# Performance work log

Measured on AMD Instinct MI355X. Metric: run time of the kernel, lower is better.

## Reference

```python
import jax, jax.numpy as jnp
import numpy as np

C = 256
INTER = 32  # C // reduction_ratio(8)
B, H, W = 4, 64, 64


def setup_inputs() -> dict:
    key = jax.random.key(0)
    ks = jax.random.split(key, 8)
    x = jax.random.normal(ks[0], (B, C, H, W), dtype=jnp.float32)
    # 1x1 conv weights stored as [out, in] matrices + biases
    Wq = jax.random.normal(ks[1], (INTER, C), dtype=jnp.float32) * (1.0 / np.sqrt(C))
    bq = jnp.zeros((INTER,), dtype=jnp.float32)
    Wk = jax.random.normal(ks[2], (INTER, C), dtype=jnp.float32) * (1.0 / np.sqrt(C))
    bk = jnp.zeros((INTER,), dtype=jnp.float32)
    Wv = jax.random.normal(ks[3], (C, C), dtype=jnp.float32) * (1.0 / np.sqrt(C))
    bv = jnp.zeros((C,), dtype=jnp.float32)
    gamma = jnp.zeros((1,), dtype=jnp.float32)
    return {"x": x, "Wq": Wq, "bq": bq, "Wk": Wk, "bk": bk, "Wv": Wv, "bv": bv, "gamma": gamma}


def reference(x, Wq, bq, Wk, bk, Wv, bv, gamma):
    b, c, h, w = x.shape
    n = h * w
    xf = x.reshape(b, c, n)  # [B,C,N]
    # 1x1 convs == channel matmuls
    q = jnp.einsum('ic,bcn->bin', Wq, xf) + bq[None, :, None]  # [B,I,N]
    k = jnp.einsum('ic,bcn->bin', Wk, xf) + bk[None, :, None]  # [B,I,N]
    v = jnp.einsum('oc,bcn->bon', Wv, xf) + bv[None, :, None]  # [B,C,N]
    scale = INTER ** (-0.5)
    attn = jnp.einsum('bin,bim->bnm', q, k) * scale  # [B,N,N]
    attn = jax.nn.softmax(attn, axis=-1)
    out = jnp.einsum('bcm,bnm->bcn', v, attn)  # value @ attn^T
    out = out.reshape(b, c, h, w)
    return gamma[0] * out + x
```

## Files before the change

kernel.cpp:

```cpp
#include <hip/hip_runtime.h>
#include <hip/hip_bf16.h>
#include <cstddef>
#include <cstdint>

#define BB 4
#define CC 256
#define II 32
#define NN 4096

#define SCALE_Q 0.25505572751402893f

typedef __attribute__((ext_vector_type(8))) short bf16x8;
typedef __attribute__((ext_vector_type(16))) float f32x16;

static __device__ __forceinline__ int cvt_pk_bf16(float lo, float hi) {
  int d;
  asm("v_cvt_pk_bf16_f32 %0, %1, %2" : "=v"(d) : "v"(lo), "v"(hi));
  return d;
}
static __device__ __forceinline__ void perm32swap_f(float& a, float& b) {
  asm("v_permlane32_swap_b32 %0, %1" : "+v"(a), "+v"(b));
}
static __device__ __forceinline__ float max3f(float a, float b, float c) {
  float d;
  asm("v_max3_f32 %0, %1, %2, %3" : "=v"(d) : "v"(a), "v"(b), "v"(c));
  return d;
}
static __device__ __forceinline__ f32x16 zero16() {
  f32x16 z;
#pragma unroll
  for (int i = 0; i < 16; ++i) z[i] = 0.0f;
  return z;
}
static __device__ __forceinline__ bf16x8 pack8(float f0, float f1, float f2,
    float f3, float f4, float f5, float f6, float f7) {
  union { int w[4]; bf16x8 v8; } u;
  u.w[0] = cvt_pk_bf16(f0, f1);
  u.w[1] = cvt_pk_bf16(f2, f3);
  u.w[2] = cvt_pk_bf16(f4, f5);
  u.w[3] = cvt_pk_bf16(f6, f7);
  return u.v8;
}
static __device__ __forceinline__ ushort f2bfu(float f) {
  union { __hip_bfloat16 h; ushort u; } cv;
  cv.h = __float2bfloat16(f);
  return cv.u;
}
static __device__ __forceinline__ int pack4_fp8(float a, float b, float c, float d) {
  int r = __builtin_amdgcn_cvt_pk_fp8_f32(a, b, 0, false);
  r = __builtin_amdgcn_cvt_pk_fp8_f32(c, d, r, true);
  return r;
}
static __device__ __forceinline__ unsigned char f2fp8(float f) {
  return (unsigned char)(__builtin_amdgcn_cvt_pk_fp8_f32(f, f, 0, false) & 0xff);
}


__global__ __launch_bounds__(64) void prepack_w(
    const float* __restrict__ Wq, const float* __restrict__ Wk,
    const float* __restrict__ Wv, ushort* __restrict__ wpre) {
  const int g = blockIdx.x;
  const int ks = blockIdx.y;
  const int lane = threadIdx.x;
  const int l31 = lane & 31;
  const int h = lane >> 5;
  const float* src = (g == 0) ? (Wq + (size_t)l31 * CC)
                   : (g == 1) ? (Wk + (size_t)l31 * CC)
                              : (Wv + (size_t)((g - 2) * 32 + l31) * CC);
  const int c = ks * 16 + h * 8;
  const float4 a = *(const float4*)(src + c);
  const float4 b = *(const float4*)(src + c + 4);
  union { ushort us[8]; int4 i4; } pk;
  pk.us[0] = f2bfu(a.x); pk.us[1] = f2bfu(a.y);
  pk.us[2] = f2bfu(a.z); pk.us[3] = f2bfu(a.w);
  pk.us[4] = f2bfu(b.x); pk.us[5] = f2bfu(b.y);
  pk.us[6] = f2bfu(b.z); pk.us[7] = f2bfu(b.w);
  *(int4*)(wpre + ((size_t)g * 16 + ks) * 512 + lane * 8) = pk.i4;
}

__global__ __launch_bounds__(320, 2) void proj_lds(
    const float* __restrict__ bq, const float* __restrict__ bk,
    const float* __restrict__ bv, const float* __restrict__ x,
    const ushort* __restrict__ wpre,
    ushort* __restrict__ qT, ushort* __restrict__ kT,
    unsigned char* __restrict__ vT8) {
  __shared__ float xs[256 * 32];

  const int tid = threadIdx.x;
  const int w = tid >> 6;
  const int lane = tid & 63;
  const int l31 = lane & 31;
  const int h = lane >> 5;
  const int b = blockIdx.x;
  const int n0 = blockIdx.y * 32;

  {
    const float* xb = x + (size_t)b * CC * NN + n0;
    for (int i = w; i < 32; i += 5) {
      const float* src = xb + (size_t)(i * 8 + (lane >> 3)) * NN + (lane & 7) * 4;
      const float4 v = *(const float4*)src;
      *(float4*)&xs[i * 256 + lane * 4] = v;
    }
  }
  __syncthreads();

  const ushort* wp0 = wpre + (size_t)((w == 0) ? 0 : (2 + (w - 1) * 2)) * 16 * 512 + lane * 8;
  const ushort* wp1 = wp0 + 16 * 512;

  f32x16 acc0 = zero16(), acc1 = zero16();
#pragma unroll 4
  for (int ks = 0; ks < 16; ++ks) {
    const int c = ks * 16 + h * 8;
    const float* xp = &xs[c * 32 + l31];
    bf16x8 xf = pack8(xp[0], xp[32], xp[64], xp[96],
                      xp[128], xp[160], xp[192], xp[224]);
    const bf16x8 wf0 = *reinterpret_cast<const bf16x8*>(wp0 + ks * 512);
    const bf16x8 wf1 = *reinterpret_cast<const bf16x8*>(wp1 + ks * 512);
    acc0 = __builtin_amdgcn_mfma_f32_32x32x16_bf16(wf0, xf, acc0, 0, 0, 0);
    acc1 = __builtin_amdgcn_mfma_f32_32x32x16_bf16(wf1, xf, acc1, 0, 0, 0);
  }

  if (w == 0) {
    ushort* qb = qT + (size_t)(b * 128 + (n0 >> 5)) * 1024;
    ushort* kb = kT + (size_t)(b * 128 + (n0 >> 5)) * 1024;
#pragma unroll
    for (int r = 0; r < 16; ++r) {
      const int i = (r & 3) + 8 * (r >> 2) + 4 * h;
      const size_t off = (size_t)(i >> 4) * 512 + ((i >> 3) & 1) * 256 + 8 * l31 + (i & 7);
      qb[off] = f2bfu((acc0[r] + bq[i]) * SCALE_Q);
      kb[off] = f2bfu(acc1[r] + bk[i]);
    }
  } else {
    const int n = n0 + l31;
    const size_t nsub = (size_t)(n >> 4) * 512 + ((size_t)((n >> 3) & 1)) * 256 + (n & 7);
    const size_t bbase = (size_t)b * (1 << 20);
#pragma unroll
    for (int r = 0; r < 16; ++r) {
      const int rp = (r & 3) + 8 * (r >> 2) + 4 * h;
      const int c0 = (w - 1) * 64 + rp;
      const int c1 = c0 + 32;
      vT8[bbase + (size_t)(c0 >> 5) * 131072 + nsub + (c0 & 31) * 8] = f2fp8(acc0[r] + bv[c0]);
      vT8[bbase + (size_t)(c1 >> 5) * 131072 + nsub + (c1 & 31) * 8] = f2fp8(acc1[r] + bv[c1]);
    }
  }
}

__global__ __launch_bounds__(512, 8) void flash_coop(
    const ushort* __restrict__ qT, const ushort* __restrict__ kT,
    const unsigned char* __restrict__ vT8, const float* __restrict__ x,
    const float* __restrict__ gamma, float* __restrict__ out) {
  __shared__ __align__(16) unsigned char pbuf[32 * 264];
  __shared__ float mlds[264];
  __shared__ float slds[264];

  const int tid = threadIdx.x;
  const int lane = tid & 63;
  const int w = tid >> 6;
  const int q = lane & 31;
  const int h = lane >> 5;

  const int wg = blockIdx.x;
  const int xcd = wg & 7;
  const int b = xcd >> 1;
  const int nt = ((xcd & 1) << 6) + (wg >> 3);
  const int n0 = nt * 32;

  const ushort* qb = qT + (size_t)(b * 128 + nt) * 1024 + lane * 8;
  const bf16x8 qf0 = *reinterpret_cast<const bf16x8*>(qb);
  const bf16x8 qf1 = *reinterpret_cast<const bf16x8*>(qb + 512);

  const ushort* ktb = kT + (size_t)b * 128 * 1024;
  const unsigned char* vtb = vT8 + ((size_t)b << 20) + (size_t)w * 131072 + lane * 8;

  f32x16 acc = zero16();
  float m_run = -1e30f, l_run = 0.0f;

  for (int it = 0; it < 16; ++it) {
    const ushort* kc = ktb + (size_t)(it * 8 + w) * 1024 + lane * 8;
    const bf16x8 kf0 = *reinterpret_cast<const bf16x8*>(kc);
    const bf16x8 kf1 = *reinterpret_cast<const bf16x8*>(kc + 512);
    f32x16 st = zero16();
    __builtin_amdgcn_s_setprio(1);
    st = __builtin_amdgcn_mfma_f32_32x32x16_bf16(kf0, qf0, st, 0, 0, 0);
    st = __builtin_amdgcn_mfma_f32_32x32x16_bf16(kf1, qf1, st, 0, 0, 0);
    __builtin_amdgcn_s_setprio(0);

    float m0 = max3f(st[0], st[1], st[2]);
    float m1 = max3f(st[3], st[4], st[5]);
    float m2 = max3f(st[6], st[7], st[8]);
    float m3 = max3f(st[9], st[10], st[11]);
    m0 = max3f(st[12], st[13], m0);
    m1 = max3f(st[14], st[15], m1);
    float mx = max3f(m0, m1, fmaxf(m2, m3));
    float sw1 = mx, sw2 = mx;
    perm32swap_f(sw1, sw2);
    const float wmax = fmaxf(sw1, sw2);
    if (lane < 32) mlds[w * 33 + q] = wmax;
    __syncthreads();

    float tmax = mlds[q];
#pragma unroll
    for (int i = 1; i < 8; ++i) tmax = fmaxf(tmax, mlds[i * 33 + q]);

    if (__any(tmax > m_run + 8.0f)) {
      const float mnew = fmaxf(m_run, tmax);
      const float f = __builtin_amdgcn_exp2f(m_run - mnew);
#pragma unroll
      for (int r = 0; r < 16; ++r) acc[r] *= f;
      l_run *= f;
      m_run = mnew;
    }

#pragma unroll
    for (int r = 0; r < 16; ++r) st[r] = __builtin_amdgcn_exp2f(st[r] - m_run);
    float s0 = ((st[0] + st[1]) + (st[2] + st[3])) +
               ((st[4] + st[5]) + (st[6] + st[7]));
    float s1 = ((st[8] + st[9]) + (st[10] + st[11])) +
               ((st[12] + st[13]) + (st[14] + st[15]));
    float pssum = s0 + s1;
    float pa = pssum, pb = pssum;
    perm32swap_f(pa, pb);
    pssum = pa + pb;
    if (lane < 32) slds[w * 33 + q] = pssum;

#pragma unroll
    for (int rg = 0; rg < 4; ++rg) {
      const int pk = pack4_fp8(st[rg * 4], st[rg * 4 + 1], st[rg * 4 + 2], st[rg * 4 + 3]);
      *reinterpret_cast<int*>(&pbuf[q * 264 + w * 32 + rg * 8 + h * 4]) = pk;
    }
    __syncthreads();

    float tsum = slds[q];
#pragma unroll
    for (int i = 1; i < 8; ++i) tsum += slds[i * 33 + q];
    l_run += tsum;

    const unsigned char* vc = vtb + (size_t)(it * 16) * 512;
    __builtin_amdgcn_s_setprio(1);
#pragma unroll
    for (int kt = 0; kt < 16; ++kt) {
      const long vf = *reinterpret_cast<const long*>(vc + (size_t)kt * 512);
      const long pfr = *reinterpret_cast<const long*>(&pbuf[q * 264 + kt * 16 + h * 8]);
      acc = __builtin_amdgcn_mfma_f32_32x32x16_fp8_fp8(vf, pfr, acc, 0, 0, 0);
    }
    __builtin_amdgcn_s_setprio(0);
  }

  const float g = gamma[0];
  const float linv = 1.0f / l_run;
#pragma unroll
  for (int r = 0; r < 16; ++r) {
    const int c = w * 32 + (r & 3) + 8 * (r >> 2) + 4 * h;
    const size_t idx = ((size_t)b * CC + c) * NN + n0 + q;
    out[idx] = g * acc[r] * linv + x[idx];
  }
}

extern "C" void kernel_launch(void* const* d_in, const int* in_sizes, int n_in,
                              void* d_out, int out_size, void* d_ws, size_t ws_size,
                              hipStream_t stream) {
  const float* x = (const float*)d_in[0];
  const float* Wq = (const float*)d_in[1];
  const float* bq = (const float*)d_in[2];
  const float* Wk = (const float*)d_in[3];
  const float* bk = (const float*)d_in[4];
  const float* Wv = (const float*)d_in[5];
  const float* bv = (const float*)d_in[6];
  const float* gamma = (const float*)d_in[7];
  float* out = (float*)d_out;

  ushort* qT = (ushort*)d_ws;
  ushort* kT = qT + (size_t)BB * 128 * 1024;
  unsigned char* vT8 = (unsigned char*)(kT + (size_t)BB * 128 * 1024);
  ushort* wpre = (ushort*)(vT8 + (size_t)BB * (1 << 20));

  prepack_w<<<dim3(10, 16), dim3(64), 0, stream>>>(Wq, Wk, Wv, wpre);
  proj_lds<<<dim3(BB, NN / 32), dim3(320), 0, stream>>>(
      bq, bk, bv, x, wpre, qT, kT, vT8);
  flash_coop<<<dim3(512), dim3(512), 0, stream>>>(
      qT, kT, vT8, x, gamma, out);
}
```

Baseline: 66.63 us.

## Split attention over key halves and merge partials in a combine kernel

Splits the flash attention key loop into two halves, doubling the workgroup count from 512 to 1024. Each half writes bf16 partial outputs plus running max and sum to workspace, and a new combine kernel rescales and merges them, then applies gamma and the residual. This targets low occupancy or under-filled CUs with only 512 workgroups. In exchange it adds a partial-output round trip (about 16 MB bf16), an extra launch, and bf16 rounding of partials. It falls back to the old kernel when the workspace is too small.

```diff
diff --git a/kernel.cpp b/kernel.cpp
--- a/kernel.cpp
+++ b/kernel.cpp
@@ -45,6 +45,11 @@
   union { __hip_bfloat16 h; ushort u; } cv;
   cv.h = __float2bfloat16(f);
   return cv.u;
+}
+static __device__ __forceinline__ float bf2f(ushort u) {
+  union { uint32_t i; float f; } cv;
+  cv.i = ((uint32_t)u) << 16;
+  return cv.f;
 }
 static __device__ __forceinline__ int pack4_fp8(float a, float b, float c, float d) {
   int r = __builtin_amdgcn_cvt_pk_fp8_f32(a, b, 0, false);
@@ -145,6 +150,150 @@
   }
 }
 
+__global__ __launch_bounds__(512, 8) void flash_split(
+    const ushort* __restrict__ qT, const ushort* __restrict__ kT,
+    const unsigned char* __restrict__ vT8,
+    ushort* __restrict__ opar, float* __restrict__ mpar,
+    float* __restrict__ lpar) {
+  __shared__ __align__(16) unsigned char pbuf[32 * 264];
+  __shared__ float mlds[264];
+  __shared__ float slds[264];
+
+  const int tid = threadIdx.x;
+  const int lane = tid & 63;
+  const int w = tid >> 6;
+  const int q = lane & 31;
+  const int h = lane >> 5;
+
+  const int wg = blockIdx.x;
+  const int xcd = wg & 7;
+  const int pos = wg >> 3;
+  const int b = xcd >> 1;
+  const int half = pos >> 6;
+  const int nt = ((xcd & 1) << 6) + (pos & 63);
+
+  const ushort* qb = qT + (size_t)(b * 128 + nt) * 1024 + lane * 8;
+  const bf16x8 qf0 = *reinterpret_cast<const bf16x8*>(qb);
+  const bf16x8 qf1 = *reinterpret_cast<const bf16x8*>(qb + 512);
+
+  const ushort* ktb = kT + (size_t)b * 128 * 1024;
+  const unsigned char* vtb = vT8 + ((size_t)b << 20) + (size_t)w * 131072 + lane * 8;
+
+  f32x16 acc = zero16();
+  float m_run = -1e30f, l_run = 0.0f;
+
+  const int it0 = half * 8;
+  for (int it = it0; it < it0 + 8; ++it) {
+    const ushort* kc = ktb + (size_t)(it * 8 + w) * 1024 + lane * 8;
+    const bf16x8 kf0 = *reinterpret_cast<const bf16x8*>(kc);
+    const bf16x8 kf1 = *reinterpret_cast<const bf16x8*>(kc + 512);
+    f32x16 st = zero16();
+    __builtin_amdgcn_s_setprio(1);
+    st = __builtin_amdgcn_mfma_f32_32x32x16_bf16(kf0, qf0, st, 0, 0, 0);
+    st = __builtin_amdgcn_mfma_f32_32x32x16_bf16(kf1, qf1, st, 0, 0, 0);
+    __builtin_amdgcn_s_setprio(0);
+
+    float m0 = max3f(st[0], st[1], st[2]);
+    float m1 = max3f(st[3], st[4], st[5]);
+    float m2 = max3f(st[6], st[7], st[8]);
+    float m3 = max3f(st[9], st[10], st[11]);
+    m0 = max3f(st[12], st[13], m0);
+    m1 = max3f(st[14], st[15], m1);
+    float mx = max3f(m0, m1, fmaxf(m2, m3));
+    float sw1 = mx, sw2 = mx;
+    perm32swap_f(sw1, sw2);
+    if (lane < 32) mlds[w * 33 + q] = fmaxf(sw1, sw2);
+    __syncthreads();
+
+    float tmax = mlds[q];
+#pragma unroll
+    for (int i = 1; i < 8; ++i) tmax = fmaxf(tmax, mlds[i * 33 + q]);
+
+    if (__any(tmax > m_run + 8.0f)) {
+      const float mnew = fmaxf(m_run, tmax);
+      const float f = __builtin_amdgcn_exp2f(m_run - mnew);
+#pragma unroll
+      for (int r = 0; r < 16; ++r) acc[r] *= f;
+      l_run *= f;
+      m_run = mnew;
+    }
+
+#pragma unroll
+    for (int r = 0; r < 16; ++r) st[r] = __builtin_amdgcn_exp2f(st[r] - m_run);
+    float s0 = ((st[0] + st[1]) + (st[2] + st[3])) +
+               ((st[4] + st[5]) + (st[6] + st[7]));
+    float s1 = ((st[8] + st[9]) + (st[10] + st[11])) +
+               ((st[12] + st[13]) + (st[14] + st[15]));
+    float pssum = s0 + s1;
+    float pa = pssum, pb = pssum;
+    perm32swap_f(pa, pb);
+    pssum = pa + pb;
+    if (lane < 32) slds[w * 33 + q] = pssum;
+
+#pragma unroll
+    for (int rg = 0; rg < 4; ++rg) {
+      const int pk = pack4_fp8(st[rg * 4], st[rg * 4 + 1], st[rg * 4 + 2], st[rg * 4 + 3]);
+      *reinterpret_cast<int*>(&pbuf[q * 264 + w * 32 + rg * 8 + h * 4]) = pk;
+    }
+    __syncthreads();
+
+    float tsum = slds[q];
+#pragma unroll
+    for (int i = 1; i < 8; ++i) tsum += slds[i * 33 + q];
+    l_run += tsum;
+
+    const unsigned char* vc = vtb + (size_t)(it * 16) * 512;
+    __builtin_amdgcn_s_setprio(1);
+#pragma unroll
+    for (int kt = 0; kt < 16; ++kt) {
+      const long vf = *reinterpret_cast<const long*>(vc + (size_t)kt * 512);
+      const long pfr = *reinterpret_cast<const long*>(&pbuf[q * 264 + kt * 16 + h * 8]);
+      acc = __builtin_amdgcn_mfma_f32_32x32x16_fp8_fp8(vf, pfr, acc, 0, 0, 0);
+    }
+    __builtin_amdgcn_s_setprio(0);
+  }
+
+  const int hb = half * 512 + b * 128 + nt;
+  ushort* od = opar + (size_t)hb * 8192;
+#pragma unroll
+  for (int r = 0; r < 16; ++r) {
+    const int c = w * 32 + (r & 3) + 8 * (r >> 2) + 4 * h;
+    od[c * 32 + q] = f2bfu(acc[r]);
+  }
+  if (w == 0 && lane < 32) {
+    mpar[hb * 32 + q] = m_run;
+    lpar[hb * 32 + q] = l_run;
+  }
+}
+
+__global__ __launch_bounds__(256) void combine_halves(
+    const ushort* __restrict__ opar, const float* __restrict__ mpar,
+    const float* __restrict__ lpar, const float* __restrict__ x,
+    const float* __restrict__ gamma, float* __restrict__ out) {
+  const int b = blockIdx.x, nt = blockIdx.y;
+  const int tid = threadIdx.x;
+  const int q = tid & 31;
+  const int c0 = tid >> 5;
+  const int i0 = (b * 128 + nt) * 32 + q;
+  const int i1 = (512 + b * 128 + nt) * 32 + q;
+  const float m0 = mpar[i0], m1 = mpar[i1];
+  const float l0 = lpar[i0], l1 = lpar[i1];
+  const float mt = fmaxf(m0, m1);
+  const float f0 = exp2f(m0 - mt), f1 = exp2f(m1 - mt);
+  const float lt = f0 * l0 + f1 * l1;
+  const float s = gamma[0] / lt;
+  const ushort* p0 = opar + (size_t)(b * 128 + nt) * 8192;
+  const ushort* p1 = opar + (size_t)(512 + b * 128 + nt) * 8192;
+#pragma unroll 4
+  for (int k = 0; k < 32; ++k) {
+    const int c = c0 + k * 8;
+    const int off = c * 32 + q;
+    const float o = f0 * bf2f(p0[off]) + f1 * bf2f(p1[off]);
+    const size_t idx = ((size_t)b * CC + c) * NN + nt * 32 + q;
+    out[idx] = s * o + x[idx];
+  }
+}
+
 __global__ __launch_bounds__(512, 8) void flash_coop(
     const ushort* __restrict__ qT, const ushort* __restrict__ kT,
     const unsigned char* __restrict__ vT8, const float* __restrict__ x,
@@ -194,8 +343,7 @@
     float mx = max3f(m0, m1, fmaxf(m2, m3));
     float sw1 = mx, sw2 = mx;
     perm32swap_f(sw1, sw2);
-    const float wmax = fmaxf(sw1, sw2);
-    if (lane < 32) mlds[w * 33 + q] = wmax;
+    if (lane < 32) mlds[w * 33 + q] = fmaxf(sw1, sw2);
     __syncthreads();
 
     float tmax = mlds[q];
@@ -270,13 +418,25 @@
   float* out = (float*)d_out;
 
   ushort* qT = (ushort*)d_ws;
-  ushort* kT = qT + (size_t)BB * 128 * 1024;
-  unsigned char* vT8 = (unsigned char*)(kT + (size_t)BB * 128 * 1024);
-  ushort* wpre = (ushort*)(vT8 + (size_t)BB * (1 << 20));
+  ushort* kT = qT + (size_t)524288;
+  unsigned char* vT8 = (unsigned char*)(kT + (size_t)524288);
+  ushort* wpre = (ushort*)(vT8 + ((size_t)1 << 22));
+  ushort* opar = wpre + 81920;
+  float* mpar = (float*)(opar + (size_t)8388608);
+  float* lpar = mpar + 32768;
+  const size_t need = (size_t)((char*)(lpar + 32768) - (char*)d_ws);
 
   prepack_w<<<dim3(10, 16), dim3(64), 0, stream>>>(Wq, Wk, Wv, wpre);
   proj_lds<<<dim3(BB, NN / 32), dim3(320), 0, stream>>>(
       bq, bk, bv, x, wpre, qT, kT, vT8);
-  flash_coop<<<dim3(512), dim3(512), 0, stream>>>(
-      qT, kT, vT8, x, gamma, out);
-}
+
+  if (ws_size >= need) {
+    flash_split<<<dim3(1024), dim3(512), 0, stream>>>(
+        qT, kT, vT8, opar, mpar, lpar);
+    combine_halves<<<dim3(BB, 128), dim3(256), 0, stream>>>(
+        opar, mpar, lpar, x, gamma, out);
+  } else {
+    flash_coop<<<dim3(512), dim3(512), 0, stream>>>(
+        qT, kT, vT8, x, gamma, out);
+  }
+}
```

Measured after the change: 72.63 us. 1.09x slower.
